# Performance work log

Measured on AMD Instinct MI355X. Metric: run time of the kernel, lower is better.

The kernel has to match this reference:

```python
import jax, jax.numpy as jnp
import numpy as np


def setup_inputs() -> dict:
    key = jax.random.key(0)
    k1, k2 = jax.random.split(key)
    # x: [B, D, H, W, C] 3D latent grid, C == embedding_dim
    x = jax.random.normal(k1, (4, 32, 32, 16, 256), dtype=jnp.float32)
    # codebook stored as (embedding_dim, num_embeddings) like the TF variable
    embeddings = jax.random.uniform(k2, (256, 4096), dtype=jnp.float32)
    return {"x": x, "embeddings": embeddings}


def reference(x, embeddings):
    # Inference-mode forward of VectorQuantizer.call (training=False).
    D, K = embeddings.shape  # (embedding_dim, num_embeddings)
    flat = x.reshape(-1, D)  # [N, D]
    # squared L2 distances: ||z||^2 + ||e||^2 - 2 z.e  -> [N, K]
    sim = flat @ embeddings
    dist = (jnp.sum(flat * flat, axis=1, keepdims=True)
            + jnp.sum(embeddings * embeddings, axis=0)
            - 2.0 * sim)
    idx = jnp.argmin(dist, axis=1)  # [N]
    # nearest-codebook lookup (gather codebook columns)
    quantized = jnp.take(embeddings.T, idx, axis=0).reshape(x.shape)
    # perplexity from code usage histogram (avoids materializing [N,K] one-hot)
    n = flat.shape[0]
    counts = jnp.zeros((K,), dtype=jnp.float32).at[idx].add(1.0)
    avg_probs = counts / n
    perplexity = jnp.exp(-jnp.sum(avg_probs * jnp.log(avg_probs + 1e-10)))
    return quantized, perplexity
```

## Files before the change

kernel.cpp:

```cpp
#include <hip/hip_runtime.h>
#include <hip/hip_bf16.h>

#define NROWS 65536
#define DIM   256
#define KCB   4096
#define CHUNK 32
#define NCH   (KCB / CHUNK)
#define NBUF  4
#define BUFB  16384
#define NENH_BASE (NBUF * BUFB)

typedef __attribute__((ext_vector_type(8))) short bf16x8;
typedef __attribute__((ext_vector_type(4))) float f32x4;

#define WAITV0 asm volatile("s_waitcnt vmcnt(0)" ::: "memory")
#define WAITV4 asm volatile("s_waitcnt vmcnt(4)" ::: "memory")
#define WAITV8 asm volatile("s_waitcnt vmcnt(8)" ::: "memory")

__device__ inline short f2bf(float f) {
    __hip_bfloat16 h = __float2bfloat16(f);
    return *reinterpret_cast<short*>(&h);
}

__global__ void prep_transpose(const float* __restrict__ E,
                               float* __restrict__ ET32,
                               ushort* __restrict__ ETbf)
{
    __shared__ float tile[64][65];
    const int kb = blockIdx.x * 64;
    const int db = blockIdx.y * 64;
    const int lo = threadIdx.x & 63;
    const int hi = threadIdx.x >> 6;

#pragma unroll
    for (int i = 0; i < 16; ++i) {
        int d = i * 4 + hi;
        tile[lo][d] = E[(size_t)(db + d) * KCB + kb + lo];
    }
    __syncthreads();
#pragma unroll
    for (int i = 0; i < 16; ++i) {
        int k = i * 4 + hi;
        float v = tile[k][lo];
        size_t off = (size_t)(kb + k) * DIM + db + lo;
        ET32[off] = v;
        ETbf[off] = (ushort)f2bf(v);
    }
}

__global__ void prep_enorm(const float* __restrict__ E, float* __restrict__ nenh)
{
    int k = blockIdx.x * 256 + threadIdx.x;
    float s = 0.0f;
#pragma unroll 8
    for (int d = 0; d < DIM; ++d) {
        float v = E[(size_t)d * KCB + k];
        s = fmaf(v, v, s);
    }
    nenh[k] = -0.5f * s;
}

__shared__ char lds_raw[NBUF * BUFB + 16384];

template <int BUF>
__device__ __forceinline__ void stage_chunk(
    const char* __restrict__ etb, const int (&soff)[4], int wave, int ct)
{
    const char* base = etb + (size_t)ct * (CHUNK * 512);
#pragma unroll
    for (int j = 0; j < 4; ++j) {
        __builtin_amdgcn_global_load_lds(
            (const __attribute__((address_space(1))) unsigned*)(base + soff[j]),
            (__attribute__((address_space(3))) unsigned*)
                (lds_raw + BUF * BUFB + wave * 4096 + j * 1024),
            16, 0, 0);
    }
}

template <int BUF>
__device__ __forceinline__ void read_batch(
    const int (&boffB)[8], int nhbyte, bf16x8 (&bfr)[8], float& nh)
{
    nh = *(const float*)(lds_raw + NENH_BASE + nhbyte);
#pragma unroll
    for (int kc = 0; kc < 8; ++kc)
        bfr[kc] = *(const bf16x8*)(lds_raw + BUF * BUFB + boffB[kc]);
}

__device__ __forceinline__ void mfma_cluster(
    const bf16x8 (&afrag)[4][8], const bf16x8 (&bfr)[8], float nh,
    unsigned (&best)[4][4], int col)
{
    f32x4 acc[4];
#pragma unroll
    for (int rt = 0; rt < 4; ++rt) acc[rt] = {nh, nh, nh, nh};
#pragma unroll
    for (int kc = 0; kc < 8; ++kc)
#pragma unroll
        for (int rt = 0; rt < 4; ++rt)
            acc[rt] = __builtin_amdgcn_mfma_f32_16x16x32_bf16(
                afrag[rt][kc], bfr[kc], acc[rt], 0, 0, 0);
#pragma unroll
    for (int rt = 0; rt < 4; ++rt)
#pragma unroll
        for (int r = 0; r < 4; ++r) {
            unsigned u = __float_as_uint(acc[rt][r]);
            unsigned key = u ^ ((unsigned)((int)u >> 31) | 0x80000000u);
            unsigned pk = (key & 0xFFFFF000u) | (unsigned)col;
            best[rt][r] = max(best[rt][r], pk);
        }
}

template <int BUF, int WN, bool STG>
__device__ __forceinline__ void chunk_step(
    const char* __restrict__ etb, const int (&soff)[4], int wave, int ct,
    const int (&boffB)[8], int hc,
    const bf16x8 (&afrag)[4][8], unsigned (&best)[4][4])
{
    if constexpr (WN == 8) { WAITV8; }
    else if constexpr (WN == 4) { WAITV4; }
    else { WAITV0; }
    __builtin_amdgcn_s_barrier();
    __builtin_amdgcn_sched_barrier(0);
    if constexpr (STG) stage_chunk<(BUF + 3) & 3>(etb, soff, wave, ct + 3);
    bf16x8 bfr[8];
    float nh;
    read_batch<BUF>(boffB, ct * 128 + hc * 4, bfr, nh);
    mfma_cluster(afrag, bfr, nh, best, ct * CHUNK + hc);
}

__global__ __launch_bounds__(256, 2)
void vq_argmin(const float* __restrict__ X,
               const ushort* __restrict__ ETbf,
               const float* __restrict__ nenh,
               int* __restrict__ idxout)
{
    const int tid  = threadIdx.x;
    const int lane = tid & 63;
    const int wave = tid >> 6;
    const int rg   = wave & 1;
    const int h    = wave >> 1;
    const int l15  = lane & 15;
    const int g    = lane >> 4;
    const int m    = l15 & 7;
    const int hc   = h * 16 + l15;
    const long rowbase = (long)blockIdx.x * 128 + rg * 64;
    const char* etb = (const char*)ETbf;

    bf16x8 afrag[4][8];
#pragma unroll
    for (int rt = 0; rt < 4; ++rt) {
        const float* xr = X + (rowbase + rt * 16 + l15) * DIM;
#pragma unroll
        for (int kc = 0; kc < 8; ++kc) {
            int k0 = g * 64 + kc * 8;
            float4 v0 = *(const float4*)(xr + k0);
            float4 v1 = *(const float4*)(xr + k0 + 4);
            bf16x8 f;
            f[0] = f2bf(v0.x); f[1] = f2bf(v0.y);
            f[2] = f2bf(v0.z); f[3] = f2bf(v0.w);
            f[4] = f2bf(v1.x); f[5] = f2bf(v1.y);
            f[6] = f2bf(v1.z); f[7] = f2bf(v1.w);
            afrag[rt][kc] = f;
        }
    }

    int soff[4];
#pragma unroll
    for (int j = 0; j < 4; ++j) {
        const int o    = wave * 4096 + j * 1024 + lane * 16;
        const int col0 = o >> 9;
        const int cph  = (o >> 4) & 31;
        soff[j] = (col0 << 9) + ((cph ^ (col0 & 7)) << 4);
    }

    int boffB[8];
#pragma unroll
    for (int kc = 0; kc < 8; ++kc)
        boffB[kc] = h * 8192 + l15 * 512 + ((((g << 3) + kc) ^ m) << 4);

#pragma unroll
    for (int j = 0; j < 4; ++j) {
        int o = wave * 4096 + j * 1024 + lane * 16;
        __builtin_amdgcn_global_load_lds(
            (const __attribute__((address_space(1))) unsigned*)((const char*)nenh + o),
            (__attribute__((address_space(3))) unsigned*)
                (lds_raw + NENH_BASE + wave * 4096 + j * 1024),
            16, 0, 0);
    }
    stage_chunk<0>(etb, soff, wave, 0);
    stage_chunk<1>(etb, soff, wave, 1);
    stage_chunk<2>(etb, soff, wave, 2);

    unsigned best[4][4];
#pragma unroll
    for (int rt = 0; rt < 4; ++rt)
#pragma unroll
        for (int r = 0; r < 4; ++r) best[rt][r] = 0u;

    for (int gq = 0; gq < 31; ++gq) {
        const int ct = gq * 4;
        chunk_step<0, 8, true>(etb, soff, wave, ct + 0, boffB, hc, afrag, best);
        chunk_step<1, 8, true>(etb, soff, wave, ct + 1, boffB, hc, afrag, best);
        chunk_step<2, 8, true>(etb, soff, wave, ct + 2, boffB, hc, afrag, best);
        chunk_step<3, 8, true>(etb, soff, wave, ct + 3, boffB, hc, afrag, best);
    }
    chunk_step<0, 8, true >(etb, soff, wave, 124, boffB, hc, afrag, best);
    chunk_step<1, 8, false>(etb, soff, wave, 125, boffB, hc, afrag, best);
    chunk_step<2, 4, false>(etb, soff, wave, 126, boffB, hc, afrag, best);
    chunk_step<3, 0, false>(etb, soff, wave, 127, boffB, hc, afrag, best);

    __syncthreads();
    unsigned* mrg = (unsigned*)lds_raw;
#pragma unroll
    for (int rt = 0; rt < 4; ++rt) {
#pragma unroll
        for (int r = 0; r < 4; ++r) {
            unsigned pk = best[rt][r];
#pragma unroll
            for (int off = 1; off < 16; off <<= 1)
                pk = max(pk, (unsigned)__shfl_xor((int)pk, off, 64));
            if (l15 == 0) {
                int row = rg * 64 + rt * 16 + g * 4 + r;
                mrg[h * 128 + row] = pk;
            }
        }
    }
    __syncthreads();
    if (tid < 128) {
        unsigned k = max(mrg[tid], mrg[128 + tid]);
        idxout[(long)blockIdx.x * 128 + tid] = (int)(k & 0xFFFu);
    }
}

__global__ void vq_gather(const int* __restrict__ idxin,
                          const float* __restrict__ ET32,
                          float* __restrict__ out,
                          unsigned* __restrict__ counts)
{
    const int tid = threadIdx.x;
    const long n  = (long)blockIdx.x * 4 + (tid >> 6);
    const int d4  = tid & 63;
    const int idx = idxin[n];
    float4 v = *(const float4*)(ET32 + (size_t)idx * DIM + d4 * 4);
    *(float4*)(out + n * DIM + d4 * 4) = v;
    if (d4 == 0) atomicAdd(&counts[idx], 1u);
}

__global__ void vq_perplexity(const unsigned* __restrict__ counts, float* __restrict__ outp)
{
    __shared__ float wsum[4];
    const int tid = threadIdx.x;
    float s = 0.0f;
    for (int k = tid; k < KCB; k += 256) {
        float p = (float)counts[k] * (1.0f / (float)NROWS);
        s += p * logf(p + 1e-10f);
    }
#pragma unroll
    for (int off = 32; off >= 1; off >>= 1) s += __shfl_down(s, off, 64);
    if ((tid & 63) == 0) wsum[tid >> 6] = s;
    __syncthreads();
    if (tid == 0) outp[0] = expf(-(wsum[0] + wsum[1] + wsum[2] + wsum[3]));
}

extern "C" void kernel_launch(void* const* d_in, const int* in_sizes, int n_in,
                              void* d_out, int out_size, void* d_ws, size_t ws_size,
                              hipStream_t stream)
{
    const float* X = (const float*)d_in[0];
    const float* E = (const float*)d_in[1];
    float* out = (float*)d_out;

    char* ws = (char*)d_ws;
    float*    ET32   = (float*)ws;
    ushort*   ETbf   = (ushort*)(ws + (size_t)KCB * DIM * 4);
    float*    nenh   = (float*)(ws + (size_t)KCB * DIM * 6);
    int*      idxbuf = (int*)(ws + (size_t)KCB * DIM * 6 + KCB * 4);
    unsigned* counts = (unsigned*)(ws + (size_t)KCB * DIM * 6 + KCB * 4 + NROWS * 4);

    hipMemsetAsync(counts, 0, KCB * sizeof(unsigned), stream);

    prep_transpose<<<dim3(KCB / 64, DIM / 64), dim3(256), 0, stream>>>(E, ET32, ETbf);
    prep_enorm<<<KCB / 256, dim3(256), 0, stream>>>(E, nenh);
    vq_argmin<<<NROWS / 128, dim3(256), 0, stream>>>(X, ETbf, nenh, idxbuf);
    vq_gather<<<NROWS / 4, dim3(256), 0, stream>>>(idxbuf, ET32, out, counts);
    vq_perplexity<<<1, dim3(256), 0, stream>>>(counts, out + (size_t)NROWS * DIM);
}
```

Before: 184.1 us.

## Replace block-wide 4-stage codebook pipeline with per-wave private double buffers

Each wave now stages its own 16-column slice of each codebook chunk into a private double-buffered LDS region. It waits only on its own outstanding loads, so the per-chunk workgroup barrier goes away. The intent is to remove the barrier stalls that made all four waves run in lockstep. In exchange, prefetch depth drops from three chunks to one, and the two waves that share a column half now each fetch the same codebook data, which doubles L2 read traffic.

```diff
diff --git a/kernel.cpp b/kernel.cpp
--- a/kernel.cpp
+++ b/kernel.cpp
@@ -6,16 +6,13 @@
 #define KCB   4096
 #define CHUNK 32
 #define NCH   (KCB / CHUNK)
-#define NBUF  4
-#define BUFB  16384
-#define NENH_BASE (NBUF * BUFB)
+#define WBUFB 8192
+#define NENH_BASE 65536
 
 typedef __attribute__((ext_vector_type(8))) short bf16x8;
 typedef __attribute__((ext_vector_type(4))) float f32x4;
 
 #define WAITV0 asm volatile("s_waitcnt vmcnt(0)" ::: "memory")
-#define WAITV4 asm volatile("s_waitcnt vmcnt(4)" ::: "memory")
-#define WAITV8 asm volatile("s_waitcnt vmcnt(8)" ::: "memory")
 
 __device__ inline short f2bf(float f) {
     __hip_bfloat16 h = __float2bfloat16(f);
@@ -60,31 +57,21 @@
     nenh[k] = -0.5f * s;
 }
 
-__shared__ char lds_raw[NBUF * BUFB + 16384];
-
-template <int BUF>
-__device__ __forceinline__ void stage_chunk(
-    const char* __restrict__ etb, const int (&soff)[4], int wave, int ct)
+__shared__ char lds_raw[4 * 2 * WBUFB + 16384];
+
+template <int PAR>
+__device__ __forceinline__ void stage_self(
+    const char* __restrict__ etb, const int (&soff)[8], int wbase, int ct)
 {
     const char* base = etb + (size_t)ct * (CHUNK * 512);
 #pragma unroll
-    for (int j = 0; j < 4; ++j) {
+    for (int j = 0; j < 8; ++j) {
         __builtin_amdgcn_global_load_lds(
             (const __attribute__((address_space(1))) unsigned*)(base + soff[j]),
             (__attribute__((address_space(3))) unsigned*)
-                (lds_raw + BUF * BUFB + wave * 4096 + j * 1024),
+                (lds_raw + wbase + PAR * WBUFB + j * 1024),
             16, 0, 0);
     }
-}
-
-template <int BUF>
-__device__ __forceinline__ void read_batch(
-    const int (&boffB)[8], int nhbyte, bf16x8 (&bfr)[8], float& nh)
-{
-    nh = *(const float*)(lds_raw + NENH_BASE + nhbyte);
-#pragma unroll
-    for (int kc = 0; kc < 8; ++kc)
-        bfr[kc] = *(const bf16x8*)(lds_raw + BUF * BUFB + boffB[kc]);
 }
 
 __device__ __forceinline__ void mfma_cluster(
@@ -111,21 +98,20 @@
         }
 }
 
-template <int BUF, int WN, bool STG>
-__device__ __forceinline__ void chunk_step(
-    const char* __restrict__ etb, const int (&soff)[4], int wave, int ct,
+template <int PAR, bool STG>
+__device__ __forceinline__ void chunk_self(
+    const char* __restrict__ etb, const int (&soff)[8], int wbase, int ct,
     const int (&boffB)[8], int hc,
     const bf16x8 (&afrag)[4][8], unsigned (&best)[4][4])
 {
-    if constexpr (WN == 8) { WAITV8; }
-    else if constexpr (WN == 4) { WAITV4; }
-    else { WAITV0; }
-    __builtin_amdgcn_s_barrier();
+    WAITV0;
     __builtin_amdgcn_sched_barrier(0);
-    if constexpr (STG) stage_chunk<(BUF + 3) & 3>(etb, soff, wave, ct + 3);
+    if constexpr (STG) stage_self<PAR ^ 1>(etb, soff, wbase, ct + 1);
+    float nh = *(const float*)(lds_raw + NENH_BASE + ct * 128 + hc * 4);
     bf16x8 bfr[8];
-    float nh;
-    read_batch<BUF>(boffB, ct * 128 + hc * 4, bfr, nh);
+#pragma unroll
+    for (int kc = 0; kc < 8; ++kc)
+        bfr[kc] = *(const bf16x8*)(lds_raw + wbase + PAR * WBUFB + boffB[kc]);
     mfma_cluster(afrag, bfr, nh, best, ct * CHUNK + hc);
 }
 
@@ -144,6 +130,7 @@
     const int g    = lane >> 4;
     const int m    = l15 & 7;
     const int hc   = h * 16 + l15;
+    const int wbase = wave * (2 * WBUFB);
     const long rowbase = (long)blockIdx.x * 128 + rg * 64;
     const char* etb = (const char*)ETbf;
 
@@ -165,19 +152,19 @@
         }
     }
 
-    int soff[4];
-#pragma unroll
-    for (int j = 0; j < 4; ++j) {
-        const int o    = wave * 4096 + j * 1024 + lane * 16;
-        const int col0 = o >> 9;
-        const int cph  = (o >> 4) & 31;
-        soff[j] = (col0 << 9) + ((cph ^ (col0 & 7)) << 4);
+    int soff[8];
+#pragma unroll
+    for (int j = 0; j < 8; ++j) {
+        const int o   = j * 1024 + lane * 16;
+        const int col = h * 16 + (o >> 9);
+        const int cph = (o >> 4) & 31;
+        soff[j] = (col << 9) + ((cph ^ (col & 7)) << 4);
     }
 
     int boffB[8];
 #pragma unroll
     for (int kc = 0; kc < 8; ++kc)
-        boffB[kc] = h * 8192 + l15 * 512 + ((((g << 3) + kc) ^ m) << 4);
+        boffB[kc] = l15 * 512 + ((((g << 3) + kc) ^ m) << 4);
 
 #pragma unroll
     for (int j = 0; j < 4; ++j) {
@@ -188,9 +175,7 @@
                 (lds_raw + NENH_BASE + wave * 4096 + j * 1024),
             16, 0, 0);
     }
-    stage_chunk<0>(etb, soff, wave, 0);
-    stage_chunk<1>(etb, soff, wave, 1);
-    stage_chunk<2>(etb, soff, wave, 2);
+    stage_self<0>(etb, soff, wbase, 0);
 
     unsigned best[4][4];
 #pragma unroll
@@ -198,17 +183,15 @@
 #pragma unroll
         for (int r = 0; r < 4; ++r) best[rt][r] = 0u;
 
-    for (int gq = 0; gq < 31; ++gq) {
-        const int ct = gq * 4;
-        chunk_step<0, 8, true>(etb, soff, wave, ct + 0, boffB, hc, afrag, best);
-        chunk_step<1, 8, true>(etb, soff, wave, ct + 1, boffB, hc, afrag, best);
-        chunk_step<2, 8, true>(etb, soff, wave, ct + 2, boffB, hc, afrag, best);
-        chunk_step<3, 8, true>(etb, soff, wave, ct + 3, boffB, hc, afrag, best);
-    }
-    chunk_step<0, 8, true >(etb, soff, wave, 124, boffB, hc, afrag, best);
-    chunk_step<1, 8, false>(etb, soff, wave, 125, boffB, hc, afrag, best);
-    chunk_step<2, 4, false>(etb, soff, wave, 126, boffB, hc, afrag, best);
-    chunk_step<3, 0, false>(etb, soff, wave, 127, boffB, hc, afrag, best);
+    WAITV0;
+    __syncthreads();
+
+    for (int c2 = 0; c2 < 63; ++c2) {
+        chunk_self<0, true>(etb, soff, wbase, c2 * 2,     boffB, hc, afrag, best);
+        chunk_self<1, true>(etb, soff, wbase, c2 * 2 + 1, boffB, hc, afrag, best);
+    }
+    chunk_self<0, true >(etb, soff, wbase, 126, boffB, hc, afrag, best);
+    chunk_self<1, false>(etb, soff, wbase, 127, boffB, hc, afrag, best);
 
     __syncthreads();
     unsigned* mrg = (unsigned*)lds_raw;
```

Measured after the change: 192.2 us. +4.4%, slower.
